# Performance work log

Measured on AMD Instinct MI355X. Metric: run time of the kernel, lower is better.

The kernel has to match this reference:

```python
import jax, jax.numpy as jnp
import numpy as np

B, IN, H, L, OUT, T, S0 = 512, 64, 512, 2, 12, 31, 8
HEAD = (T - 1) / 2  # 15.0
EPS = 1e-5


def setup_inputs() -> dict:
    key = jax.random.key(0)
    ks = jax.random.split(key, 10)
    s = 0.05
    return {
        "Wih0": jax.random.normal(ks[0], (4 * H, IN), jnp.float32) * s,
        "Whh0": jax.random.normal(ks[1], (4 * H, H), jnp.float32) * s,
        "b0": jax.random.normal(ks[2], (4 * H,), jnp.float32) * s,
        "Wih1": jax.random.normal(ks[3], (4 * H, H), jnp.float32) * s,
        "Whh1": jax.random.normal(ks[4], (4 * H, H), jnp.float32) * s,
        "b1": jax.random.normal(ks[5], (4 * H,), jnp.float32) * s,
        "gamma": jnp.ones((H,), jnp.float32),
        "beta": jnp.zeros((H,), jnp.float32),
        "Wout": jax.random.normal(ks[6], (OUT, H), jnp.float32) * s,
        "bout": jax.random.normal(ks[7], (OUT,), jnp.float32) * s,
        "h0": jax.random.uniform(ks[8], (L, H), jnp.float32),
        "c0": jax.random.uniform(ks[9], (L, H), jnp.float32),
    }


def _lstm_layer(xs, h0, c0, Wih, Whh, b):
    # xs: (B, d_in) treated as an unbatched sequence of length B (torch semantics here).
    def step(carry, x):
        h, c = carry
        g = x @ Wih.T + h @ Whh.T + b  # (4H,)
        i, f, gg, o = jnp.split(g, 4, axis=-1)  # torch gate order: i, f, g, o
        c = jax.nn.sigmoid(f) * c + jax.nn.sigmoid(i) * jnp.tanh(gg)
        h = jax.nn.sigmoid(o) * jnp.tanh(c)
        return (h, c), h
    (hT, cT), ys = jax.lax.scan(step, (h0, c0), xs)
    return ys, hT, cT


def reference(Wih0, Whh0, b0, Wih1, Whh1, b1, gamma, beta, Wout, bout, h0, c0):
    keys = jax.random.split(jax.random.key(42), T)
    x = jnp.ones((B, IN), jnp.float32)
    h, c = h0, c0  # (L, H)
    acts, lps = [], []
    for i in range(T):
        ys0, h0n, c0n = _lstm_layer(x, h[0], c[0], Wih0, Whh0, b0)
        ys1, h1n, c1n = _lstm_layer(ys0, h[1], c[1], Wih1, Whh1, b1)
        h = jnp.stack([h0n, h1n])
        c = jnp.stack([c0n, c1n])
        # BatchNorm1d, training mode (biased variance over the B dim)
        mu = ys1.mean(0)
        var = ys1.var(0)
        yn = (ys1 - mu) / jnp.sqrt(var + EPS) * gamma + beta
        g = jnp.exp(-yn ** 2)  # GaussianActivation
        logits = g @ Wout.T + bout  # (B, OUT)
        if i < HEAD:
            action = jax.random.categorical(keys[i], logits, axis=-1)
        else:
            action = jax.random.categorical(keys[i], logits[:, S0:], axis=-1) + S0
        # log_prob under the FULL categorical (as in the original code)
        lp = jax.nn.log_softmax(logits, axis=-1)[jnp.arange(B), action]
        acts.append(action)
        lps.append(lp)
    return jnp.stack(acts), jnp.stack(lps)  # ((T,B) int, (T,B) float)
```

## Files before the change

kernel.cpp:

```cpp
#include <hip/hip_runtime.h>
#include <stdint.h>
#include <math.h>

#define Bv      512
#define INv     64
#define Hv      512
#define OUTv    12
#define Tv      31
#define S0v     8
#define STEPS   (Tv*Bv)

#define KA      16
#define KB      32
#define KPP     16
#define NBLK    (KA+KB+KPP)
#define RING    32


__device__ __forceinline__ uint32_t rotl32(uint32_t v, int r){ return (v<<r)|(v>>(32-r)); }

__device__ __forceinline__ void threefry2x32(uint32_t k0, uint32_t k1,
                                             uint32_t x0, uint32_t x1,
                                             uint32_t& o0, uint32_t& o1) {
  uint32_t ks2 = k0 ^ k1 ^ 0x1BD11BDAu;
  x0 += k0; x1 += k1;
#define TFR(r) { x0 += x1; x1 = rotl32(x1, r); x1 ^= x0; }
  TFR(13) TFR(15) TFR(26) TFR(6)
  x0 += k1;  x1 += ks2 + 1u;
  TFR(17) TFR(29) TFR(16) TFR(24)
  x0 += ks2; x1 += k0 + 2u;
  TFR(13) TFR(15) TFR(26) TFR(6)
  x0 += k0;  x1 += k1 + 3u;
  TFR(17) TFR(29) TFR(16) TFR(24)
  x0 += k1;  x1 += ks2 + 4u;
  TFR(13) TFR(15) TFR(26) TFR(6)
  x0 += ks2; x1 += k0 + 5u;
#undef TFR
  o0 = x0; o1 = x1;
}

__device__ __forceinline__ uint32_t tf_bits32(uint32_t k0, uint32_t k1, uint32_t j) {
  uint32_t a, b;
  threefry2x32(k0, k1, 0u, j, a, b);
  return a ^ b;
}

__device__ __forceinline__ float u32_to_uniform(uint32_t bits) {
  float f = __uint_as_float(0x3F800000u | (bits >> 9)) - 1.0f;
  const float TINY = 1.17549435e-38f;
  return fmaxf(TINY, f + TINY);
}

__device__ __forceinline__ float gumbelf(uint32_t bits) {
  float u = u32_to_uniform(bits);
  return -logf(-logf(u));
}

__device__ __forceinline__ float sigmf(float x) {
  if (x >= 0.f) { float z = expf(-x); return 1.f/(1.f+z); }
  float z = expf(x); return z/(1.f+z);
}

template<int N>
__device__ __forceinline__ void bfly_halve(float* v, int m) {
  int lane = threadIdx.x & 63;
  bool up = (lane & m) != 0;
#pragma unroll
  for (int j = 0; j < N/2; ++j) {
    float send = up ? v[j] : v[j + N/2];
    float recv = __shfl_xor(send, m, 64);
    v[j] = (up ? v[j + N/2] : v[j]) + recv;
  }
}

__device__ __forceinline__ uint64_t aload64(const uint64_t* p){
  return __hip_atomic_load(p, __ATOMIC_RELAXED, __HIP_MEMORY_SCOPE_AGENT);
}
__device__ __forceinline__ void astore64(uint64_t* p, uint64_t v){
  __hip_atomic_store(p, v, __ATOMIC_RELAXED, __HIP_MEMORY_SCOPE_AGENT);
}
__device__ __forceinline__ uint32_t aload32(const uint32_t* p){
  return __hip_atomic_load(p, __ATOMIC_RELAXED, __HIP_MEMORY_SCOPE_AGENT);
}
__device__ __forceinline__ void astore32(uint32_t* p, uint32_t v){
  __hip_atomic_store(p, v, __ATOMIC_RELAXED, __HIP_MEMORY_SCOPE_AGENT);
}
__device__ __forceinline__ uint32_t tagof(uint64_t w){ return (uint32_t)(w>>32); }
__device__ __forceinline__ float    valof(uint64_t w){ return __uint_as_float((uint32_t)w); }
__device__ __forceinline__ uint64_t mkword(uint32_t t, float v){
  return ((uint64_t)t<<32) | (uint64_t)__float_as_uint(v);
}

__device__ __forceinline__ uint64_t spin_eq(const uint64_t* p, uint64_t lo, uint64_t hi) {
  uint64_t q0, q1, sc;
  asm volatile(
    "global_load_dwordx2 %[q0], %[ap], off sc0 sc1\n\t"
    "global_load_dwordx2 %[q1], %[ap], off sc0 sc1\n\t"
    "1:\n\t"
    "s_waitcnt vmcnt(1)\n\t"
    "v_cmp_lt_u64 vcc, %[q0], %[lo]\n\t"
    "v_cmp_ge_u64 %[sc], %[q0], %[hi]\n\t"
    "s_or_b64 vcc, vcc, %[sc]\n\t"
    "s_cbranch_vccz 2f\n\t"
    "global_load_dwordx2 %[q0], %[ap], off sc0 sc1\n\t"
    "s_sleep 1\n\t"
    "s_waitcnt vmcnt(1)\n\t"
    "v_cmp_lt_u64 vcc, %[q1], %[lo]\n\t"
    "v_cmp_ge_u64 %[sc], %[q1], %[hi]\n\t"
    "s_or_b64 vcc, vcc, %[sc]\n\t"
    "s_cbranch_vccz 3f\n\t"
    "global_load_dwordx2 %[q1], %[ap], off sc0 sc1\n\t"
    "s_sleep 1\n\t"
    "s_branch 1b\n\t"
    "3:\n\t"
    "s_waitcnt vmcnt(0)\n\t"
    "v_lshlrev_b64 %[q0], 0, %[q1]\n\t"
    "2:\n\t"
    "s_waitcnt vmcnt(0)\n\t"
    : [q0]"=&v"(q0), [q1]"=&v"(q1), [sc]"=&s"(sc)
    : [ap]"v"(p), [lo]"v"(lo), [hi]"v"(hi)
    : "vcc", "memory");
  return q0;
}

__device__ __forceinline__ void spin_xy(const uint64_t* px, const uint64_t* py,
                                        uint64_t lo, uint64_t hi,
                                        uint64_t& xr, uint64_t& yr) {
  uint64_t x, q0, q1, sc;
  asm volatile(
    "global_load_dwordx2 %[x],  %[xp], off sc0 sc1\n\t"
    "global_load_dwordx2 %[q0], %[yp], off sc0 sc1\n\t"
    "global_load_dwordx2 %[q1], %[yp], off sc0 sc1\n\t"
    "1:\n\t"
    "s_waitcnt vmcnt(1)\n\t"
    "v_cmp_lt_u64 vcc, %[q0], %[lo]\n\t"
    "v_cmp_ge_u64 %[sc], %[q0], %[hi]\n\t"
    "s_or_b64 vcc, vcc, %[sc]\n\t"
    "s_cbranch_vccz 2f\n\t"
    "global_load_dwordx2 %[q0], %[yp], off sc0 sc1\n\t"
    "s_sleep 1\n\t"
    "s_waitcnt vmcnt(1)\n\t"
    "v_cmp_lt_u64 vcc, %[q1], %[lo]\n\t"
    "v_cmp_ge_u64 %[sc], %[q1], %[hi]\n\t"
    "s_or_b64 vcc, vcc, %[sc]\n\t"
    "s_cbranch_vccz 3f\n\t"
    "global_load_dwordx2 %[q1], %[yp], off sc0 sc1\n\t"
    "s_sleep 1\n\t"
    "s_branch 1b\n\t"
    "3:\n\t"
    "s_waitcnt vmcnt(0)\n\t"
    "v_lshlrev_b64 %[q0], 0, %[q1]\n\t"
    "2:\n\t"
    "s_waitcnt vmcnt(0)\n\t"
    : [x]"=&v"(x), [q0]"=&v"(q0), [q1]"=&v"(q1), [sc]"=&s"(sc)
    : [xp]"v"(px), [yp]"v"(py), [lo]"v"(lo), [hi]"v"(hi)
    : "vcc", "memory");
  xr = x; yr = q0;
}

__global__ __launch_bounds__(512, 1)
void net_persistent(const float* __restrict__ Wih0, const float* __restrict__ Whh0,
                    const float* __restrict__ b0,
                    const float* __restrict__ Wih1, const float* __restrict__ Whh1,
                    const float* __restrict__ b1,
                    const float* __restrict__ gamma, const float* __restrict__ beta,
                    const float* __restrict__ Wout, const float* __restrict__ bout,
                    const float* __restrict__ h0in, const float* __restrict__ c0in,
                    float* __restrict__ out, uint32_t* __restrict__ wsu)
{
  uint32_t* iterflag = wsu;
  uint64_t* h0A = (uint64_t*)((char*)wsu + 4096);
  uint64_t* h0B = (uint64_t*)((char*)wsu + 4096 + (size_t)RING*Hv*8);
  uint64_t* y1c = (uint64_t*)((char*)wsu + 4096 + (size_t)2*RING*Hv*8);
  float*    ys1 = (float*)((char*)wsu + 4096 + (size_t)3*RING*Hv*8);

  const int bid  = blockIdx.x;
  const int tid  = threadIdx.x;
  const int wave = tid >> 6;
  const int lane = tid & 63;

  __shared__ float hbuf[2][Hv];
  __shared__ float xbuf[2][2*Hv];
  __shared__ float pub_s[32];
  __shared__ float Wout_s[OUTv*Hv];
  __shared__ float mu_s[Hv], isd_s[Hv], gam_s[Hv], bet_s[Hv];

  if (bid < KA) {
    const int hbase = bid*32;
    float w[128];
#pragma unroll
    for (int jl = 0; jl < 4; ++jl)
#pragma unroll
      for (int g = 0; g < 4; ++g) {
        int r = jl*4 + g;
        const float* rp = Whh0 + (size_t)(g*Hv + hbase + wave*4 + jl)*Hv;
#pragma unroll
        for (int k = 0; k < 2; ++k) {
          float4 q = *(const float4*)(rp + k*256 + lane*4);
          w[r*8+k*4+0]=q.x; w[r*8+k*4+1]=q.y; w[r*8+k*4+2]=q.z; w[r*8+k*4+3]=q.w;
        }
      }
    const int jsel = lane & 3;
    const int hg = hbase + wave*4 + jsel;
    float cgi, cgf, cgg, cgo;
    {
      float s0=b0[0*Hv+hg], s1=b0[1*Hv+hg], s2=b0[2*Hv+hg], s3=b0[3*Hv+hg];
      for (int k = 0; k < INv; ++k) {
        s0 += Wih0[(size_t)(0*Hv+hg)*INv+k];
        s1 += Wih0[(size_t)(1*Hv+hg)*INv+k];
        s2 += Wih0[(size_t)(2*Hv+hg)*INv+k];
        s3 += Wih0[(size_t)(3*Hv+hg)*INv+k];
      }
      cgi=s0; cgf=s1; cgg=s2; cgo=s3;
    }
    float cst = c0in[hg];

    for (int s = 0; s < STEPS; ++s) {
      const int par = s & 1;
      if ((s & 15) == 0 && s >= 32) {
        const uint64_t* tp = y1c + (size_t)((s-17)&(RING-1))*Hv + lane*8;
        uint32_t need = (uint32_t)(s - 16);
        for (;;) {
          uint32_t t = tagof(aload64(tp));
          if (__all((int)(t >= need && t <= (uint32_t)STEPS))) break;
          __builtin_amdgcn_s_sleep(1);
        }
      }
      if (s == 0) {
        hbuf[0][tid] = h0in[tid];
      } else {
        const uint64_t* src = h0A + (size_t)((s-1)&(RING-1))*Hv + tid;
        uint64_t lo = (uint64_t)(uint32_t)s << 32;
        uint64_t a = spin_eq(src, lo, lo + (1ull << 32));
        hbuf[par][tid] = valof(a);
      }
      __syncthreads();
      const float4* hv = (const float4*)(hbuf[par]);
      float4 vA = hv[lane], vB = hv[64 + lane];
      float acc[16];
#pragma unroll
      for (int r = 0; r < 16; ++r) {
        float a = 0.f;
        a = fmaf(w[r*8+0], vA.x, a); a = fmaf(w[r*8+1], vA.y, a);
        a = fmaf(w[r*8+2], vA.z, a); a = fmaf(w[r*8+3], vA.w, a);
        a = fmaf(w[r*8+4], vB.x, a); a = fmaf(w[r*8+5], vB.y, a);
        a = fmaf(w[r*8+6], vB.z, a); a = fmaf(w[r*8+7], vB.w, a);
        acc[r] = a;
      }
      bfly_halve<16>(acc, 32);
      bfly_halve<8>(acc, 16);
      bfly_halve<4>(acc, 8);
      bfly_halve<2>(acc, 4);
      acc[0] += __shfl_xor(acc[0], 2, 64);
      acc[0] += __shfl_xor(acc[0], 1, 64);
      float gi = __shfl(acc[0], 16*jsel + 0,  64);
      float gf = __shfl(acc[0], 16*jsel + 4,  64);
      float gg = __shfl(acc[0], 16*jsel + 8,  64);
      float go = __shfl(acc[0], 16*jsel + 12, 64);
      float cc = sigmf(gf+cgf)*cst + sigmf(gi+cgi)*tanhf(gg+cgg);
      float hh = sigmf(go+cgo)*tanhf(cc);
      cst = cc;
      if (lane < 4) pub_s[wave*4 + lane] = hh;
      __syncthreads();
      if (wave < 2 && lane < 32) {
        uint64_t* dst = (wave == 0) ? h0A : h0B;
        astore64(dst + (size_t)(s&(RING-1))*Hv + hbase + lane,
                 mkword((uint32_t)(s+1), pub_s[lane]));
      }
    }
  } else if (bid < KA + KB) {
    const int wg1 = bid - KA;
    const int hbase = wg1*16;
    float w[128];
#pragma unroll
    for (int jl = 0; jl < 2; ++jl)
#pragma unroll
      for (int g = 0; g < 4; ++g) {
        int r = jl*4 + g;
        int row = g*Hv + hbase + wave*2 + jl;
#pragma unroll
        for (int k = 0; k < 4; ++k) {
          int col = k*256 + lane*4;
          const float* M = (col < Hv) ? (Wih1 + (size_t)row*Hv + col)
                                      : (Whh1 + (size_t)row*Hv + (col - Hv));
          float4 q = *(const float4*)M;
          w[r*16+k*4+0]=q.x; w[r*16+k*4+1]=q.y; w[r*16+k*4+2]=q.z; w[r*16+k*4+3]=q.w;
        }
      }
    const int jsel = lane & 1;
    const int hg = hbase + wave*2 + jsel;
    float cgi = b1[0*Hv+hg], cgf = b1[1*Hv+hg],
          cgg = b1[2*Hv+hg], cgo = b1[3*Hv+hg];
    float cst = c0in[Hv + hg];

    for (int s = 0; s < STEPS; ++s) {
      const int par = s & 1;
      {
        const uint64_t* px = h0B + (size_t)(s&(RING-1))*Hv + tid;
        const uint32_t wantx = (uint32_t)(s+1);
        if (s == 0) {
          uint64_t lox = (uint64_t)wantx << 32;
          uint64_t x = spin_eq(px, lox, lox + (1ull << 32));
          xbuf[0][tid]      = valof(x);
          xbuf[0][Hv + tid] = h0in[Hv + tid];
        } else {
          const uint64_t* py = y1c + (size_t)((s-1)&(RING-1))*Hv + tid;
          uint64_t lo = (uint64_t)(uint32_t)s << 32;
          uint64_t x, y;
          spin_xy(px, py, lo, lo + (1ull << 32), x, y);
          while (tagof(x) != wantx) x = aload64(px);
          xbuf[par][tid]      = valof(x);
          xbuf[par][Hv + tid] = valof(y);
        }
      }
      __syncthreads();
      const float4* xv = (const float4*)(xbuf[par]);
      float4 v0 = xv[lane], v1 = xv[64+lane], v2 = xv[128+lane], v3 = xv[192+lane];
      float acc[8];
#pragma unroll
      for (int r = 0; r < 8; ++r) {
        float a = 0.f;
        a = fmaf(w[r*16+ 0], v0.x, a); a = fmaf(w[r*16+ 1], v0.y, a);
        a = fmaf(w[r*16+ 2], v0.z, a); a = fmaf(w[r*16+ 3], v0.w, a);
        a = fmaf(w[r*16+ 4], v1.x, a); a = fmaf(w[r*16+ 5], v1.y, a);
        a = fmaf(w[r*16+ 6], v1.z, a); a = fmaf(w[r*16+ 7], v1.w, a);
        a = fmaf(w[r*16+ 8], v2.x, a); a = fmaf(w[r*16+ 9], v2.y, a);
        a = fmaf(w[r*16+10], v2.z, a); a = fmaf(w[r*16+11], v2.w, a);
        a = fmaf(w[r*16+12], v3.x, a); a = fmaf(w[r*16+13], v3.y, a);
        a = fmaf(w[r*16+14], v3.z, a); a = fmaf(w[r*16+15], v3.w, a);
        acc[r] = a;
      }
      bfly_halve<8>(acc, 32);
      bfly_halve<4>(acc, 16);
      bfly_halve<2>(acc, 8);
      acc[0] += __shfl_xor(acc[0], 4, 64);
      acc[0] += __shfl_xor(acc[0], 2, 64);
      acc[0] += __shfl_xor(acc[0], 1, 64);
      float gi = __shfl(acc[0], 32*jsel + 0,  64);
      float gf = __shfl(acc[0], 32*jsel + 8,  64);
      float gg = __shfl(acc[0], 32*jsel + 16, 64);
      float go = __shfl(acc[0], 32*jsel + 24, 64);
      float cc = sigmf(gf+cgf)*cst + sigmf(gi+cgi)*tanhf(gg+cgg);
      float hh = sigmf(go+cgo)*tanhf(cc);
      cst = cc;
      if (lane < 2) pub_s[wave*2 + lane] = hh;
      __syncthreads();
      if (wave == 0 && lane < 16) {
        astore64(y1c + (size_t)(s&(RING-1))*Hv + hbase + lane,
                 mkword((uint32_t)(s+1), pub_s[lane]));
      } else if (wave == 1 && lane < 16) {
        ys1[(size_t)s*Hv + hbase + lane] = pub_s[lane];
      }
      if ((s & 511) == 511) {
        __syncthreads();
        if (tid == 0) {
          __builtin_amdgcn_fence(__ATOMIC_RELEASE, "agent");
          astore32(iterflag + wg1, (uint32_t)((s >> 9) + 1));
        }
      }
    }
  } else {
    const int p = bid - KA - KB;
    for (int r = tid; r < OUTv*Hv; r += 512) Wout_s[r] = Wout[r];
    for (int h = tid; h < Hv; h += 512) { gam_s[h] = gamma[h]; bet_s[h] = beta[h]; }
    float bo[OUTv];
#pragma unroll
    for (int o = 0; o < OUTv; ++o) bo[o] = bout[o];
    __syncthreads();

    for (int i = p; i < Tv; i += KPP) {
      const uint32_t tgt = (uint32_t)(i + 1);
      if (tid < 64) {
        for (;;) {
          uint32_t v = aload32(iterflag + (lane & 31));
          if (__all((int)(v >= tgt && v <= (uint32_t)Tv))) break;
          __builtin_amdgcn_s_sleep(16);
        }
      }
      __syncthreads();
      __builtin_amdgcn_fence(__ATOMIC_ACQUIRE, "agent");

      const float* Y = ys1 + (size_t)i * Bv * Hv;

      for (int h = tid; h < Hv; h += 512) {
        double sum = 0.0, sq = 0.0;
        for (int b = 0; b < Bv; ++b) {
          double v = (double)Y[(size_t)b*Hv + h];
          sum += v; sq += v*v;
        }
        double mu = sum * (1.0/512.0);
        double var = sq * (1.0/512.0) - mu*mu;
        if (var < 0.0) var = 0.0;
        mu_s[h]  = (float)mu;
        isd_s[h] = (float)(1.0 / sqrt(var + 1e-5));
      }
      __syncthreads();

      uint32_t k0, k1;
      threefry2x32(0u, 42u, 0u, (uint32_t)i, k0, k1);

      for (int b = tid; b < Bv; b += 512) {
        float lg[OUTv];
#pragma unroll
        for (int o = 0; o < OUTv; ++o) lg[o] = 0.f;
        const float* Yb = Y + (size_t)b * Hv;
        for (int h = 0; h < Hv; ++h) {
          float yn = (Yb[h] - mu_s[h]) * isd_s[h] * gam_s[h] + bet_s[h];
          float gv = expf(-yn*yn);
#pragma unroll
          for (int o = 0; o < OUTv; ++o) lg[o] = fmaf(gv, Wout_s[o*Hv + h], lg[o]);
        }
#pragma unroll
        for (int o = 0; o < OUTv; ++o) lg[o] += bo[o];

        int action; float la;
        if (i < 15) {
          float best = -3.0e38f; int bi = 0; float bl = lg[0];
#pragma unroll
          for (int o = 0; o < OUTv; ++o) {
            uint32_t bits = tf_bits32(k0, k1, (uint32_t)(b*12 + o));
            float z = gumbelf(bits) + lg[o];
            if (z > best) { best = z; bi = o; bl = lg[o]; }
          }
          action = bi; la = bl;
        } else {
          float best = -3.0e38f; int bi = 0; float bl = lg[S0v];
#pragma unroll
          for (int o = 0; o < 4; ++o) {
            uint32_t bits = tf_bits32(k0, k1, (uint32_t)(b*4 + o));
            float z = gumbelf(bits) + lg[S0v + o];
            if (z > best) { best = z; bi = o; bl = lg[S0v + o]; }
          }
          action = S0v + bi; la = bl;
        }

        float mx = lg[0];
#pragma unroll
        for (int o = 1; o < OUTv; ++o) mx = fmaxf(mx, lg[o]);
        float se = 0.f;
#pragma unroll
        for (int o = 0; o < OUTv; ++o) se += expf(lg[o] - mx);
        float lp = (la - mx) - logf(se);

        out[i*Bv + b]         = (float)action;
        out[STEPS + i*Bv + b] = lp;
      }
    }
  }
}

extern "C" void kernel_launch(void* const* d_in, const int* in_sizes, int n_in,
                              void* d_out, int out_size, void* d_ws, size_t ws_size,
                              hipStream_t stream) {
  const float* Wih0 = (const float*)d_in[0];
  const float* Whh0 = (const float*)d_in[1];
  const float* b0   = (const float*)d_in[2];
  const float* Wih1 = (const float*)d_in[3];
  const float* Whh1 = (const float*)d_in[4];
  const float* b1   = (const float*)d_in[5];
  const float* gam  = (const float*)d_in[6];
  const float* bet  = (const float*)d_in[7];
  const float* Wout = (const float*)d_in[8];
  const float* bout = (const float*)d_in[9];
  const float* h0   = (const float*)d_in[10];
  const float* c0   = (const float*)d_in[11];

  net_persistent<<<dim3(NBLK), dim3(512), 0, stream>>>(
      Wih0, Whh0, b0, Wih1, Whh1, b1, gam, bet, Wout, bout, h0, c0,
      (float*)d_out, (uint32_t*)d_ws);
}
```

Baseline: 34.90 ms.

## Use 1024-thread blocks and halve LSTM block counts to cut cross-block syncs

Doubles the block size to 1024 threads and halves the number of layer-0 and layer-1 blocks, so each block owns twice as many hidden units. Fewer blocks take part in the per-step global-memory flag handshake, which is meant to cut cross-CU synchronisation latency on the sequential recurrence. In layer 1 the x and y inputs are now fetched by separate thread halves instead of through a combined spin routine. The risk is the heavier per-block work, the larger __syncthreads cost, and register pressure at 1024 threads with 128 weight registers per thread.

```diff
diff --git a/kernel.cpp b/kernel.cpp
--- a/kernel.cpp
+++ b/kernel.cpp
@@ -10,8 +10,8 @@
 #define S0v     8
 #define STEPS   (Tv*Bv)
 
-#define KA      16
-#define KB      32
+#define KA      8
+#define KB      16
 #define KPP     16
 #define NBLK    (KA+KB+KPP)
 #define RING    32
@@ -123,42 +123,7 @@
   return q0;
 }
 
-__device__ __forceinline__ void spin_xy(const uint64_t* px, const uint64_t* py,
-                                        uint64_t lo, uint64_t hi,
-                                        uint64_t& xr, uint64_t& yr) {
-  uint64_t x, q0, q1, sc;
-  asm volatile(
-    "global_load_dwordx2 %[x],  %[xp], off sc0 sc1\n\t"
-    "global_load_dwordx2 %[q0], %[yp], off sc0 sc1\n\t"
-    "global_load_dwordx2 %[q1], %[yp], off sc0 sc1\n\t"
-    "1:\n\t"
-    "s_waitcnt vmcnt(1)\n\t"
-    "v_cmp_lt_u64 vcc, %[q0], %[lo]\n\t"
-    "v_cmp_ge_u64 %[sc], %[q0], %[hi]\n\t"
-    "s_or_b64 vcc, vcc, %[sc]\n\t"
-    "s_cbranch_vccz 2f\n\t"
-    "global_load_dwordx2 %[q0], %[yp], off sc0 sc1\n\t"
-    "s_sleep 1\n\t"
-    "s_waitcnt vmcnt(1)\n\t"
-    "v_cmp_lt_u64 vcc, %[q1], %[lo]\n\t"
-    "v_cmp_ge_u64 %[sc], %[q1], %[hi]\n\t"
-    "s_or_b64 vcc, vcc, %[sc]\n\t"
-    "s_cbranch_vccz 3f\n\t"
-    "global_load_dwordx2 %[q1], %[yp], off sc0 sc1\n\t"
-    "s_sleep 1\n\t"
-    "s_branch 1b\n\t"
-    "3:\n\t"
-    "s_waitcnt vmcnt(0)\n\t"
-    "v_lshlrev_b64 %[q0], 0, %[q1]\n\t"
-    "2:\n\t"
-    "s_waitcnt vmcnt(0)\n\t"
-    : [x]"=&v"(x), [q0]"=&v"(q0), [q1]"=&v"(q1), [sc]"=&s"(sc)
-    : [xp]"v"(px), [yp]"v"(py), [lo]"v"(lo), [hi]"v"(hi)
-    : "vcc", "memory");
-  xr = x; yr = q0;
-}
-
-__global__ __launch_bounds__(512, 1)
+__global__ __launch_bounds__(1024, 1)
 void net_persistent(const float* __restrict__ Wih0, const float* __restrict__ Whh0,
                     const float* __restrict__ b0,
                     const float* __restrict__ Wih1, const float* __restrict__ Whh1,
@@ -181,12 +146,12 @@
 
   __shared__ float hbuf[2][Hv];
   __shared__ float xbuf[2][2*Hv];
-  __shared__ float pub_s[32];
+  __shared__ float pub_s[64];
   __shared__ float Wout_s[OUTv*Hv];
   __shared__ float mu_s[Hv], isd_s[Hv], gam_s[Hv], bet_s[Hv];
 
   if (bid < KA) {
-    const int hbase = bid*32;
+    const int hbase = bid*64;
     float w[128];
 #pragma unroll
     for (int jl = 0; jl < 4; ++jl)
@@ -227,8 +192,8 @@
         }
       }
       if (s == 0) {
-        hbuf[0][tid] = h0in[tid];
-      } else {
+        if (tid < Hv) hbuf[0][tid] = h0in[tid];
+      } else if (tid < Hv) {
         const uint64_t* src = h0A + (size_t)((s-1)&(RING-1))*Hv + tid;
         uint64_t lo = (uint64_t)(uint32_t)s << 32;
         uint64_t a = spin_eq(src, lo, lo + (1ull << 32));
@@ -262,7 +227,7 @@
       cst = cc;
       if (lane < 4) pub_s[wave*4 + lane] = hh;
       __syncthreads();
-      if (wave < 2 && lane < 32) {
+      if (wave < 2) {
         uint64_t* dst = (wave == 0) ? h0A : h0B;
         astore64(dst + (size_t)(s&(RING-1))*Hv + hbase + lane,
                  mkword((uint32_t)(s+1), pub_s[lane]));
@@ -270,7 +235,7 @@
     }
   } else if (bid < KA + KB) {
     const int wg1 = bid - KA;
-    const int hbase = wg1*16;
+    const int hbase = wg1*32;
     float w[128];
 #pragma unroll
     for (int jl = 0; jl < 2; ++jl)
@@ -295,22 +260,19 @@
 
     for (int s = 0; s < STEPS; ++s) {
       const int par = s & 1;
-      {
+      if (tid < Hv) {
         const uint64_t* px = h0B + (size_t)(s&(RING-1))*Hv + tid;
-        const uint32_t wantx = (uint32_t)(s+1);
+        uint64_t lo = (uint64_t)(uint32_t)(s+1) << 32;
+        uint64_t x = spin_eq(px, lo, lo + (1ull << 32));
+        xbuf[par][tid] = valof(x);
+      } else {
         if (s == 0) {
-          uint64_t lox = (uint64_t)wantx << 32;
-          uint64_t x = spin_eq(px, lox, lox + (1ull << 32));
-          xbuf[0][tid]      = valof(x);
-          xbuf[0][Hv + tid] = h0in[Hv + tid];
+          xbuf[0][tid] = h0in[tid];
         } else {
-          const uint64_t* py = y1c + (size_t)((s-1)&(RING-1))*Hv + tid;
+          const uint64_t* py = y1c + (size_t)((s-1)&(RING-1))*Hv + (tid - Hv);
           uint64_t lo = (uint64_t)(uint32_t)s << 32;
-          uint64_t x, y;
-          spin_xy(px, py, lo, lo + (1ull << 32), x, y);
-          while (tagof(x) != wantx) x = aload64(px);
-          xbuf[par][tid]      = valof(x);
-          xbuf[par][Hv + tid] = valof(y);
+          uint64_t y = spin_eq(py, lo, lo + (1ull << 32));
+          xbuf[par][tid] = valof(y);
         }
       }
       __syncthreads();
@@ -345,10 +307,10 @@
       cst = cc;
       if (lane < 2) pub_s[wave*2 + lane] = hh;
       __syncthreads();
-      if (wave == 0 && lane < 16) {
+      if (wave == 0 && lane < 32) {
         astore64(y1c + (size_t)(s&(RING-1))*Hv + hbase + lane,
                  mkword((uint32_t)(s+1), pub_s[lane]));
-      } else if (wave == 1 && lane < 16) {
+      } else if (wave == 1 && lane < 32) {
         ys1[(size_t)s*Hv + hbase + lane] = pub_s[lane];
       }
       if ((s & 511) == 511) {
@@ -361,8 +323,8 @@
     }
   } else {
     const int p = bid - KA - KB;
-    for (int r = tid; r < OUTv*Hv; r += 512) Wout_s[r] = Wout[r];
-    for (int h = tid; h < Hv; h += 512) { gam_s[h] = gamma[h]; bet_s[h] = beta[h]; }
+    for (int r = tid; r < OUTv*Hv; r += 1024) Wout_s[r] = Wout[r];
+    for (int h = tid; h < Hv; h += 1024) { gam_s[h] = gamma[h]; bet_s[h] = beta[h]; }
     float bo[OUTv];
 #pragma unroll
     for (int o = 0; o < OUTv; ++o) bo[o] = bout[o];
@@ -372,7 +334,7 @@
       const uint32_t tgt = (uint32_t)(i + 1);
       if (tid < 64) {
         for (;;) {
-          uint32_t v = aload32(iterflag + (lane & 31));
+          uint32_t v = aload32(iterflag + (lane & 15));
           if (__all((int)(v >= tgt && v <= (uint32_t)Tv))) break;
           __builtin_amdgcn_s_sleep(16);
         }
@@ -382,7 +344,7 @@
 
       const float* Y = ys1 + (size_t)i * Bv * Hv;
 
-      for (int h = tid; h < Hv; h += 512) {
+      for (int h = tid; h < Hv; h += 1024) {
         double sum = 0.0, sq = 0.0;
         for (int b = 0; b < Bv; ++b) {
           double v = (double)Y[(size_t)b*Hv + h];
@@ -399,7 +361,7 @@
       uint32_t k0, k1;
       threefry2x32(0u, 42u, 0u, (uint32_t)i, k0, k1);
 
-      for (int b = tid; b < Bv; b += 512) {
+      for (int b = tid; b < Bv; b += 1024) {
         float lg[OUTv];
 #pragma unroll
         for (int o = 0; o < OUTv; ++o) lg[o] = 0.f;
@@ -465,7 +427,7 @@
   const float* h0   = (const float*)d_in[10];
   const float* c0   = (const float*)d_in[11];
 
-  net_persistent<<<dim3(NBLK), dim3(512), 0, stream>>>(
+  net_persistent<<<dim3(NBLK), dim3(1024), 0, stream>>>(
       Wih0, Whh0, b0, Wih1, Whh1, b1, gam, bet, Wout, bout, h0, c0,
       (float*)d_out, (uint32_t*)d_ws);
 }
```

Result: slower. 120.5 ms (+245.3%).
